# Kernel optimization log

Hardware: AMD Instinct MI355X
Metric: run time of the kernel (lower is better)

The kernel has to match this reference:

```python
import jax, jax.numpy as jnp
import numpy as np

B, S, H = 2, 2048, 2048
NH, NKV, HD = 16, 4, 128
THETA = 1000000.0

def _rope_tables(seq_len, dim, theta):
    inv_freq = 1.0 / (theta ** (np.arange(0, dim, 2, dtype=np.float32) / dim))
    t = np.arange(seq_len, dtype=np.float32)
    freqs = np.outer(t, inv_freq)                      # [S, dim/2]
    emb = np.concatenate([freqs, freqs], axis=-1)      # [S, dim]
    return jnp.asarray(np.cos(emb)), jnp.asarray(np.sin(emb))

def setup_inputs() -> dict:
    key = jax.random.key(0)
    ks = jax.random.split(key, 5)
    cos, sin = _rope_tables(S, HD, THETA)
    scale = 1.0 / np.sqrt(H)
    return {
        "x": jax.random.normal(ks[0], (B, S, H), jnp.float32),
        "cos": cos, "sin": sin,
        "wq": jax.random.normal(ks[1], (H, NH * HD), jnp.float32) * scale,
        "wk": jax.random.normal(ks[2], (H, NKV * HD), jnp.float32) * scale,
        "wv": jax.random.normal(ks[3], (H, NKV * HD), jnp.float32) * scale,
        "wo": jax.random.normal(ks[4], (NH * HD, H), jnp.float32) * scale,
    }

def _rotate_half(t):
    h = t.shape[-1] // 2
    return jnp.concatenate([-t[..., h:], t[..., :h]], axis=-1)

def reference(x, cos, sin, wq, wk, wv, wo):
    b, s, _ = x.shape
    n_rep = NH // NKV
    q = (x @ wq).reshape(b, s, NH, HD)    # [b,s,nh,hd]
    k = (x @ wk).reshape(b, s, NKV, HD)
    v = (x @ wv).reshape(b, s, NKV, HD)
    # RoPE: cos/sin [s,hd] broadcast over batch and heads
    c = cos[None, :, None, :]
    sn = sin[None, :, None, :]
    q = q * c + _rotate_half(q) * sn
    k = k * c + _rotate_half(k) * sn
    # GQA: repeat kv heads n_rep times
    k = jnp.repeat(k, n_rep, axis=2)      # [b,s,nh,hd]
    v = jnp.repeat(v, n_rep, axis=2)
    q = q.transpose(0, 2, 1, 3)           # [b,nh,s,hd]
    k = k.transpose(0, 2, 1, 3)
    v = v.transpose(0, 2, 1, 3)
    scores = jnp.einsum('bhqd,bhkd->bhqk', q, k) / jnp.sqrt(jnp.float32(HD))
    causal = jnp.tril(jnp.ones((s, s), dtype=bool))
    scores = jnp.where(causal[None, None], scores, jnp.float32(-jnp.inf))
    attn = jax.nn.softmax(scores.astype(jnp.float32), axis=-1).astype(q.dtype)
    out = jnp.einsum('bhqk,bhkd->bhqd', attn, v)
    out = out.transpose(0, 2, 1, 3).reshape(b, s, NH * HD)
    return out @ wo
```

## Files before the change

### kernel.cpp

```cpp
#include <hip/hip_runtime.h>
#include <hip/hip_bf16.h>

#define Bb 2
#define Ss 2048
#define Hh 2048
#define NH 16
#define NKV 4
#define HD 128
#define NREP (NH / NKV)
#define Mrows (Bb * Ss)
#define NQKV (NH*HD + 2*NKV*HD)

using short8 = __attribute__((ext_vector_type(8))) short;
using f32x4  = __attribute__((ext_vector_type(4))) float;

__device__ __forceinline__ unsigned short f2b(float f) {
  union { float f; unsigned u; } v; v.f = f;
  return (unsigned short)((v.u + 0x7fffu + ((v.u >> 16) & 1u)) >> 16);
}

__device__ __forceinline__ void gload16(const void* g, void* l) {
  __builtin_amdgcn_global_load_lds(
      (const __attribute__((address_space(1))) unsigned int*)g,
      (__attribute__((address_space(3))) unsigned int*)l, 16, 0, 0);
}

__global__ void cvt_bf16(const float* __restrict__ in, unsigned short* __restrict__ out, int n) {
  int i = (blockIdx.x * blockDim.x + threadIdx.x) * 4;
  if (i < n) {
    float4 f = *(const float4*)(in + i);
    ushort4 o;
    o.x = f2b(f.x); o.y = f2b(f.y); o.z = f2b(f.z); o.w = f2b(f.w);
    *(ushort4*)(out + i) = o;
  }
}

__global__ void transpose_cvt(const float* __restrict__ in, unsigned short* __restrict__ out,
                              int R, int C) {
  __shared__ float tile[32][33];
  int c0 = blockIdx.x * 32, r0 = blockIdx.y * 32;
  int tx = threadIdx.x, ty = threadIdx.y;
  #pragma unroll
  for (int i = ty; i < 32; i += 8)
    tile[i][tx] = in[(long)(r0 + i) * C + c0 + tx];
  __syncthreads();
  #pragma unroll
  for (int i = ty; i < 32; i += 8)
    out[(long)(c0 + i) * R + r0 + tx] = f2b(tile[tx][i]);
}

__global__ void transpose_qkv(const float* __restrict__ wq, const float* __restrict__ wk,
                              const float* __restrict__ wv, unsigned short* __restrict__ outT) {
  __shared__ float tile[32][33];
  int n0 = blockIdx.x * 32, k0 = blockIdx.y * 32;
  const float* src; int c0, C;
  if (n0 < Hh)            { src = wq; c0 = n0;            C = NH * HD; }
  else if (n0 < Hh + 512) { src = wk; c0 = n0 - Hh;       C = NKV * HD; }
  else                    { src = wv; c0 = n0 - Hh - 512; C = NKV * HD; }
  int tx = threadIdx.x, ty = threadIdx.y;
  #pragma unroll
  for (int i = ty; i < 32; i += 8)
    tile[i][tx] = src[(long)(k0 + i) * C + c0 + tx];
  __syncthreads();
  #pragma unroll
  for (int i = ty; i < 32; i += 8)
    outT[(long)(n0 + i) * Hh + k0 + tx] = f2b(tile[tx][i]);
}

__global__ __launch_bounds__(256) void gemm_qkv(const unsigned short* __restrict__ A,
                                                const unsigned short* __restrict__ Bt,
                                                const float* __restrict__ cosT,
                                                const float* __restrict__ sinT,
                                                unsigned short* __restrict__ qt,
                                                unsigned short* __restrict__ kt,
                                                unsigned short* __restrict__ vt) {
  __shared__ unsigned short As[128 * 32];
  __shared__ unsigned short Bs[128 * 32];
  const int t = threadIdx.x;
  const int lane = t & 63, wave = t >> 6;
  const int quad = lane >> 4, l16 = lane & 15;
  const int tile = blockIdx.x;
  const int n0 = tile * 128, m0 = blockIdx.y * 128;
  const int wm = wave * 32;
  const bool isv = tile >= 20;
  const int Kk = Hh;

  f32x4 acc[2][8] = {};

  const unsigned short* Ag0 = A + (long)(m0 + (t >> 2)) * Kk + (t & 3) * 8;
  const unsigned short* Ag1 = A + (long)(m0 + 64 + (t >> 2)) * Kk + (t & 3) * 8;
  const unsigned short* Bg0 = Bt + (long)(n0 + (t >> 2)) * Kk + (t & 3) * 8;
  const unsigned short* Bg1 = Bt + (long)(n0 + 64 + (t >> 2)) * Kk + (t & 3) * 8;
  unsigned short* lA0 = As + (wave * 64) * 8;
  unsigned short* lA1 = As + (wave * 64 + 256) * 8;
  unsigned short* lB0 = Bs + (wave * 64) * 8;
  unsigned short* lB1 = Bs + (wave * 64 + 256) * 8;

  for (int k0 = 0; k0 < Kk; k0 += 32) {
    gload16(Ag0 + k0, lA0);
    gload16(Ag1 + k0, lA1);
    gload16(Bg0 + k0, lB0);
    gload16(Bg1 + k0, lB1);
    __syncthreads();

    short8 af[2], bf[8];
    #pragma unroll
    for (int i = 0; i < 2; i++)
      af[i] = *(const short8*)(As + (wm + i * 16 + l16) * 32 + quad * 8);
    #pragma unroll
    for (int i = 0; i < 8; i++)
      bf[i] = *(const short8*)(Bs + (i * 16 + l16) * 32 + quad * 8);

    if (isv) {
      #pragma unroll
      for (int mi = 0; mi < 2; mi++)
        #pragma unroll
        for (int ni = 0; ni < 8; ni++)
          acc[mi][ni] = __builtin_amdgcn_mfma_f32_16x16x32_bf16(bf[ni], af[mi], acc[mi][ni], 0, 0, 0);
    } else {
      #pragma unroll
      for (int mi = 0; mi < 2; mi++)
        #pragma unroll
        for (int ni = 0; ni < 8; ni++)
          acc[mi][ni] = __builtin_amdgcn_mfma_f32_16x16x32_bf16(af[mi], bf[ni], acc[mi][ni], 0, 0, 0);
    }
    __syncthreads();
  }

  if (!isv) {
    const bool isq = tile < 16;
    const int hh = isq ? tile : tile - 16;
    #pragma unroll
    for (int mi = 0; mi < 2; mi++)
      #pragma unroll
      for (int r = 0; r < 4; r++) {
        int srow = m0 + wm + mi * 16 + quad * 4 + r;
        int bb = srow >> 11, s = srow & (Ss - 1);
        unsigned short* dst = isq ? qt + (((long)bb * NH + hh) * Ss + s) * HD
                                  : kt + (((long)bb * NKV + hh) * Ss + s) * HD;
        const float* cr = cosT + (long)s * HD;
        const float* sr = sinT + (long)s * HD;
        #pragma unroll
        for (int ni = 0; ni < 4; ni++) {
          int d = ni * 16 + l16;
          float cc = cr[d], sn = sr[d];
          float x0 = acc[mi][ni][r], x1 = acc[mi][ni + 4][r];
          dst[d]      = f2b(x0 * cc - x1 * sn);
          dst[d + 64] = f2b(x1 * cc + x0 * sn);
        }
      }
  } else {
    const int kvh = tile - 20;
    const int bb = m0 >> 11;
    #pragma unroll
    for (int mi = 0; mi < 2; mi++)
      #pragma unroll
      for (int ni = 0; ni < 8; ni++)
        #pragma unroll
        for (int r = 0; r < 4; r++) {
          int d = ni * 16 + quad * 4 + r;
          int s = (m0 + wm + mi * 16 + l16) & (Ss - 1);
          vt[(((long)bb * NKV + kvh) * HD + d) * Ss + s] = f2b(acc[mi][ni][r]);
        }
  }
}

__global__ __launch_bounds__(256) void gemm_bt(const unsigned short* __restrict__ A,
                                               const unsigned short* __restrict__ Bt,
                                               float* __restrict__ Cv,
                                               int Mm, int Nn, int Kk) {
  __shared__ unsigned short As[128 * 32];
  __shared__ unsigned short Bs[128 * 32];
  const int t = threadIdx.x;
  const int lane = t & 63, wave = t >> 6;
  const int quad = lane >> 4, l16 = lane & 15;
  const int m0 = blockIdx.y * 128, n0 = blockIdx.x * 128;
  const int wm = (wave >> 1) * 64, wn = (wave & 1) * 64;

  f32x4 acc[4][4] = {};

  const unsigned short* Ag0 = A + (long)(m0 + (t >> 2)) * Kk + (t & 3) * 8;
  const unsigned short* Ag1 = A + (long)(m0 + 64 + (t >> 2)) * Kk + (t & 3) * 8;
  const unsigned short* Bg0 = Bt + (long)(n0 + (t >> 2)) * Kk + (t & 3) * 8;
  const unsigned short* Bg1 = Bt + (long)(n0 + 64 + (t >> 2)) * Kk + (t & 3) * 8;
  unsigned short* lA0 = As + (wave * 64) * 8;
  unsigned short* lA1 = As + (wave * 64 + 256) * 8;
  unsigned short* lB0 = Bs + (wave * 64) * 8;
  unsigned short* lB1 = Bs + (wave * 64 + 256) * 8;

  for (int k0 = 0; k0 < Kk; k0 += 32) {
    gload16(Ag0 + k0, lA0);
    gload16(Ag1 + k0, lA1);
    gload16(Bg0 + k0, lB0);
    gload16(Bg1 + k0, lB1);
    __syncthreads();

    short8 af[4], bf[4];
    #pragma unroll
    for (int i = 0; i < 4; i++)
      af[i] = *(const short8*)(As + (wm + i * 16 + l16) * 32 + quad * 8);
    #pragma unroll
    for (int i = 0; i < 4; i++)
      bf[i] = *(const short8*)(Bs + (wn + i * 16 + l16) * 32 + quad * 8);

    #pragma unroll
    for (int mi = 0; mi < 4; mi++)
      #pragma unroll
      for (int ni = 0; ni < 4; ni++)
        acc[mi][ni] = __builtin_amdgcn_mfma_f32_16x16x32_bf16(af[mi], bf[ni], acc[mi][ni], 0, 0, 0);
    __syncthreads();
  }

  #pragma unroll
  for (int mi = 0; mi < 4; mi++)
    #pragma unroll
    for (int ni = 0; ni < 4; ni++)
      #pragma unroll
      for (int r = 0; r < 4; r++) {
        long row = m0 + wm + mi * 16 + quad * 4 + r;
        long col = n0 + wn + ni * 16 + l16;
        Cv[row * Nn + col] = acc[mi][ni][r];
      }
}

__global__ __launch_bounds__(256, 2) void flash_attn(const unsigned short* __restrict__ qt,
                                                     const unsigned short* __restrict__ kt,
                                                     const unsigned short* __restrict__ vt,
                                                     unsigned short* __restrict__ out) {
  __shared__ unsigned short Ks[2][64 * 128];
  __shared__ unsigned short Vs[2][128 * 64];

  const int w = threadIdx.x >> 6, lane = threadIdx.x & 63;
  const int quad = lane >> 4, l16 = lane & 15;
  const int r8 = lane >> 3, c8 = lane & 7;
  const int idx = blockIdx.x;
  const int t5 = idx >> 5;
  const int qblk = (idx < 256) ? (15 - t5) : (t5 - 8);
  const int bh = idx & 31;
  const int h = bh & (NH - 1), b = bh >> 4;
  const int q0w = qblk * 128 + w * 32;
  const int kvh = h / NREP;

  const unsigned short* Qb = qt + ((long)b * NH + h) * Ss * HD;
  const unsigned short* Kb = kt + ((long)b * NKV + kvh) * Ss * HD;
  const unsigned short* Vb = vt + ((long)b * NKV + kvh) * HD * Ss;
  const int nch = (qblk + 1) * 2;

  #pragma unroll
  for (int i = 0; i < 4; i++) {
    int rho = i * 16 + w * 4 + quad;
    int key = (rho & 32) + ((rho >> 2) & 3) * 8 + ((rho >> 4) & 1) * 4 + (rho & 3);
    int sg = l16 ^ (w * 4 + quad);
    gload16(Kb + (long)key * HD + sg * 8, &Ks[0][(i * 256 + w * 64) * 8]);
  }
  #pragma unroll
  for (int i = 0; i < 4; i++) {
    int dv = i * 32 + w * 8 + r8;
    int sg = c8 ^ r8;
    gload16(Vb + (long)dv * Ss + sg * 8, &Vs[0][(i * 256 + w * 64) * 8]);
  }

  short8 qf[2][4];
  #pragma unroll
  for (int qi = 0; qi < 2; qi++)
    #pragma unroll
    for (int kc = 0; kc < 4; kc++)
      qf[qi][kc] = *(const short8*)(Qb + (long)(q0w + qi * 16 + l16) * HD + kc * 32 + quad * 8);

  f32x4 accO[2][8] = {};
  float m_i[2], l_i[2];
  m_i[0] = m_i[1] = -__builtin_inff();
  l_i[0] = l_i[1] = 0.f;
  const float cscale = 1.4426950408889634f * 0.08838834764831845f;

  for (int c = 0; c < nch; ++c) {
    const unsigned short* Ksb = Ks[c & 1];
    const unsigned short* Vsb = Vs[c & 1];

    if (c + 1 < nch) {
      const int k0 = (c + 1) * 64;
      unsigned short* Kd = Ks[(c + 1) & 1];
      unsigned short* Vd = Vs[(c + 1) & 1];
      #pragma unroll
      for (int i = 0; i < 4; i++) {
        int rho = i * 16 + w * 4 + quad;
        int key = (rho & 32) + ((rho >> 2) & 3) * 8 + ((rho >> 4) & 1) * 4 + (rho & 3);
        int sg = l16 ^ (w * 4 + quad);
        gload16(Kb + (long)(k0 + key) * HD + sg * 8, Kd + (i * 256 + w * 64) * 8);
      }
      #pragma unroll
      for (int i = 0; i < 4; i++) {
        int dv = i * 32 + w * 8 + r8;
        int sg = c8 ^ r8;
        gload16(Vb + (long)dv * Ss + k0 + sg * 8, Vd + (i * 256 + w * 64) * 8);
      }
      asm volatile("s_waitcnt vmcnt(8)" ::: "memory");
    } else {
      asm volatile("s_waitcnt vmcnt(0)" ::: "memory");
    }
    asm volatile("s_barrier" ::: "memory");

    if (c * 64 < q0w + 32) {
      f32x4 sc[2][4] = {};
      #pragma unroll
      for (int T = 0; T < 4; T++)
        #pragma unroll
        for (int kc = 0; kc < 4; kc++) {
          short8 kf = *(const short8*)(Ksb + ((16 * T + l16) * 16 + ((kc * 4 + quad) ^ l16)) * 8);
          #pragma unroll
          for (int qi = 0; qi < 2; qi++)
            sc[qi][T] = __builtin_amdgcn_mfma_f32_16x16x32_bf16(kf, qf[qi][kc], sc[qi][T], 0, 0, 0);
        }

      if ((c + 1) * 64 - 1 > q0w) {
        #pragma unroll
        for (int qi = 0; qi < 2; qi++) {
          int qq = q0w + qi * 16 + l16;
          #pragma unroll
          for (int T = 0; T < 4; T++)
            #pragma unroll
            for (int r = 0; r < 4; r++) {
              int ka = c * 64 + (T >> 1) * 32 + quad * 8 + (T & 1) * 4 + r;
              if (ka > qq) sc[qi][T][r] = -__builtin_inff();
            }
        }
      }

      short8 pf[2][2];
      #pragma unroll
      for (int qi = 0; qi < 2; qi++) {
        float v = sc[qi][0][0];
        #pragma unroll
        for (int T = 0; T < 4; T++)
          #pragma unroll
          for (int r = 0; r < 4; r++) v = fmaxf(v, sc[qi][T][r]);
        v = fmaxf(v, __shfl_xor(v, 16));
        v = fmaxf(v, __shfl_xor(v, 32));
        float mn = fmaxf(m_i[qi], v);
        float alpha = __builtin_amdgcn_exp2f((m_i[qi] - mn) * cscale);
        m_i[qi] = mn;
        l_i[qi] *= alpha;
        #pragma unroll
        for (int Dt = 0; Dt < 8; Dt++)
          #pragma unroll
          for (int r = 0; r < 4; r++) accO[qi][Dt][r] *= alpha;

        float p[4][4], rs = 0.f;
        #pragma unroll
        for (int T = 0; T < 4; T++)
          #pragma unroll
          for (int r = 0; r < 4; r++) {
            p[T][r] = __builtin_amdgcn_exp2f((sc[qi][T][r] - mn) * cscale);
            rs += p[T][r];
          }
        rs += __shfl_xor(rs, 16);
        rs += __shfl_xor(rs, 32);
        l_i[qi] += rs;

        #pragma unroll
        for (int c2 = 0; c2 < 2; c2++) {
          short8 f;
          f[0] = (short)f2b(p[2 * c2][0]);     f[1] = (short)f2b(p[2 * c2][1]);
          f[2] = (short)f2b(p[2 * c2][2]);     f[3] = (short)f2b(p[2 * c2][3]);
          f[4] = (short)f2b(p[2 * c2 + 1][0]); f[5] = (short)f2b(p[2 * c2 + 1][1]);
          f[6] = (short)f2b(p[2 * c2 + 1][2]); f[7] = (short)f2b(p[2 * c2 + 1][3]);
          pf[qi][c2] = f;
        }
      }

      #pragma unroll
      for (int c2 = 0; c2 < 2; c2++)
        #pragma unroll
        for (int Dt = 0; Dt < 8; Dt++) {
          short8 vf = *(const short8*)(Vsb + ((16 * Dt + l16) * 8 + ((4 * c2 + quad) ^ (l16 & 7))) * 8);
          #pragma unroll
          for (int qi = 0; qi < 2; qi++)
            accO[qi][Dt] = __builtin_amdgcn_mfma_f32_16x16x32_bf16(vf, pf[qi][c2], accO[qi][Dt], 0, 0, 0);
        }
    }

    asm volatile("s_waitcnt lgkmcnt(0)" ::: "memory");
    asm volatile("s_barrier" ::: "memory");
  }

  #pragma unroll
  for (int qi = 0; qi < 2; qi++) {
    float inv = 1.f / l_i[qi];
    long orow = (long)b * Ss + q0w + qi * 16 + l16;
    #pragma unroll
    for (int Dt = 0; Dt < 8; Dt++) {
      ushort4 o;
      o.x = f2b(accO[qi][Dt][0] * inv);
      o.y = f2b(accO[qi][Dt][1] * inv);
      o.z = f2b(accO[qi][Dt][2] * inv);
      o.w = f2b(accO[qi][Dt][3] * inv);
      *(ushort4*)(out + orow * (NH * HD) + h * HD + Dt * 16 + quad * 4) = o;
    }
  }
}

extern "C" void kernel_launch(void* const* d_in, const int* in_sizes, int n_in,
                              void* d_out, int out_size, void* d_ws, size_t ws_size,
                              hipStream_t stream) {
  const float* x    = (const float*)d_in[0];
  const float* cosT = (const float*)d_in[1];
  const float* sinT = (const float*)d_in[2];
  const float* wq   = (const float*)d_in[3];
  const float* wk   = (const float*)d_in[4];
  const float* wv   = (const float*)d_in[5];
  const float* wo   = (const float*)d_in[6];
  float* out = (float*)d_out;

  char* ws = (char*)d_ws;
  unsigned short* xb    = (unsigned short*)(ws);
  unsigned short* wqkvt = (unsigned short*)(ws + (16l << 20));
  unsigned short* wot   = (unsigned short*)(ws + (28l << 20));
  unsigned short* qt    = (unsigned short*)(ws + (36l << 20));
  unsigned short* kt    = (unsigned short*)(ws + (52l << 20));
  unsigned short* vt    = (unsigned short*)(ws + (56l << 20));
  unsigned short* attno = xb;

  cvt_bf16<<<Mrows * Hh / 4 / 256, 256, 0, stream>>>(x, xb, Mrows * Hh);

  dim3 tb(32, 8);
  transpose_qkv<<<dim3(NQKV / 32, Hh / 32), tb, 0, stream>>>(wq, wk, wv, wqkvt);
  transpose_cvt<<<dim3(Hh / 32, Hh / 32), tb, 0, stream>>>(wo, wot, Hh, Hh);

  gemm_qkv<<<dim3(NQKV / 128, Mrows / 128), 256, 0, stream>>>(xb, wqkvt, cosT, sinT, qt, kt, vt);

  flash_attn<<<(Ss / 128) * NH * Bb, 256, 0, stream>>>(qt, kt, vt, attno);

  gemm_bt<<<dim3(Hh / 128, Mrows / 128), 256, 0, stream>>>(attno, wot, out, Mrows, Hh, Hh);
}
```

Baseline: 351.6 us.

## Double GEMM K-tile to 64 with XOR-swizzled LDS and column-major block order

Both bf16 GEMMs (QKV projection and output projection) now load a 64-wide K slice per iteration instead of 32. This halves the number of barrier pairs and global-load issue rounds. LDS rows are XOR-swizzled on 16-byte granules so the wider rows do not cause bank conflicts on the MFMA operand reads. The 2D grid is flattened so consecutive blocks walk down M for a fixed N tile, which is meant to improve L2 reuse of the weight tile. The cost is double the LDS per block (32 KB), which could lower occupancy.

```diff
diff --git a/kernel.cpp b/kernel.cpp
--- a/kernel.cpp
+++ b/kernel.cpp
@@ -74,55 +74,58 @@
                                                 unsigned short* __restrict__ qt,
                                                 unsigned short* __restrict__ kt,
                                                 unsigned short* __restrict__ vt) {
-  __shared__ unsigned short As[128 * 32];
-  __shared__ unsigned short Bs[128 * 32];
+  __shared__ unsigned short As[128 * 64];
+  __shared__ unsigned short Bs[128 * 64];
   const int t = threadIdx.x;
   const int lane = t & 63, wave = t >> 6;
   const int quad = lane >> 4, l16 = lane & 15;
-  const int tile = blockIdx.x;
-  const int n0 = tile * 128, m0 = blockIdx.y * 128;
+  const int tile = blockIdx.x >> 5;
+  const int n0 = tile * 128, m0 = (blockIdx.x & 31) * 128;
   const int wm = wave * 32;
   const bool isv = tile >= 20;
   const int Kk = Hh;
 
   f32x4 acc[2][8] = {};
 
-  const unsigned short* Ag0 = A + (long)(m0 + (t >> 2)) * Kk + (t & 3) * 8;
-  const unsigned short* Ag1 = A + (long)(m0 + 64 + (t >> 2)) * Kk + (t & 3) * 8;
-  const unsigned short* Bg0 = Bt + (long)(n0 + (t >> 2)) * Kk + (t & 3) * 8;
-  const unsigned short* Bg1 = Bt + (long)(n0 + 64 + (t >> 2)) * Kk + (t & 3) * 8;
-  unsigned short* lA0 = As + (wave * 64) * 8;
-  unsigned short* lA1 = As + (wave * 64 + 256) * 8;
-  unsigned short* lB0 = Bs + (wave * 64) * 8;
-  unsigned short* lB1 = Bs + (wave * 64 + 256) * 8;
-
-  for (int k0 = 0; k0 < Kk; k0 += 32) {
-    gload16(Ag0 + k0, lA0);
-    gload16(Ag1 + k0, lA1);
-    gload16(Bg0 + k0, lB0);
-    gload16(Bg1 + k0, lB1);
+  const int srow = t >> 3;
+  const int sgr  = (t & 7) ^ (srow & 7);
+  const unsigned short* Ag = A  + (long)(m0 + srow) * Kk + sgr * 8;
+  const unsigned short* Bg = Bt + (long)(n0 + srow) * Kk + sgr * 8;
+  unsigned short* lA = As + (wave * 64) * 8;
+  unsigned short* lB = Bs + (wave * 64) * 8;
+
+  for (int k0 = 0; k0 < Kk; k0 += 64) {
+    #pragma unroll
+    for (int i = 0; i < 4; i++)
+      gload16(Ag + (long)i * 32 * Kk + k0, lA + i * 256 * 8);
+    #pragma unroll
+    for (int i = 0; i < 4; i++)
+      gload16(Bg + (long)i * 32 * Kk + k0, lB + i * 256 * 8);
     __syncthreads();
 
-    short8 af[2], bf[8];
-    #pragma unroll
-    for (int i = 0; i < 2; i++)
-      af[i] = *(const short8*)(As + (wm + i * 16 + l16) * 32 + quad * 8);
-    #pragma unroll
-    for (int i = 0; i < 8; i++)
-      bf[i] = *(const short8*)(Bs + (i * 16 + l16) * 32 + quad * 8);
-
-    if (isv) {
-      #pragma unroll
-      for (int mi = 0; mi < 2; mi++)
-        #pragma unroll
-        for (int ni = 0; ni < 8; ni++)
-          acc[mi][ni] = __builtin_amdgcn_mfma_f32_16x16x32_bf16(bf[ni], af[mi], acc[mi][ni], 0, 0, 0);
-    } else {
-      #pragma unroll
-      for (int mi = 0; mi < 2; mi++)
-        #pragma unroll
-        for (int ni = 0; ni < 8; ni++)
-          acc[mi][ni] = __builtin_amdgcn_mfma_f32_16x16x32_bf16(af[mi], bf[ni], acc[mi][ni], 0, 0, 0);
+    #pragma unroll
+    for (int sub = 0; sub < 2; sub++) {
+      short8 af[2], bf[8];
+      #pragma unroll
+      for (int i = 0; i < 2; i++)
+        af[i] = *(const short8*)(As + (wm + i * 16 + l16) * 64 + (((sub * 4 + quad) ^ (l16 & 7)) * 8));
+      #pragma unroll
+      for (int i = 0; i < 8; i++)
+        bf[i] = *(const short8*)(Bs + (i * 16 + l16) * 64 + (((sub * 4 + quad) ^ (l16 & 7)) * 8));
+
+      if (isv) {
+        #pragma unroll
+        for (int mi = 0; mi < 2; mi++)
+          #pragma unroll
+          for (int ni = 0; ni < 8; ni++)
+            acc[mi][ni] = __builtin_amdgcn_mfma_f32_16x16x32_bf16(bf[ni], af[mi], acc[mi][ni], 0, 0, 0);
+      } else {
+        #pragma unroll
+        for (int mi = 0; mi < 2; mi++)
+          #pragma unroll
+          for (int ni = 0; ni < 8; ni++)
+            acc[mi][ni] = __builtin_amdgcn_mfma_f32_16x16x32_bf16(af[mi], bf[ni], acc[mi][ni], 0, 0, 0);
+      }
     }
     __syncthreads();
   }
@@ -134,8 +137,8 @@
     for (int mi = 0; mi < 2; mi++)
       #pragma unroll
       for (int r = 0; r < 4; r++) {
-        int srow = m0 + wm + mi * 16 + quad * 4 + r;
-        int bb = srow >> 11, s = srow & (Ss - 1);
+        int srw = m0 + wm + mi * 16 + quad * 4 + r;
+        int bb = srw >> 11, s = srw & (Ss - 1);
         unsigned short* dst = isq ? qt + (((long)bb * NH + hh) * Ss + s) * HD
                                   : kt + (((long)bb * NKV + hh) * Ss + s) * HD;
         const float* cr = cosT + (long)s * HD;
@@ -169,45 +172,48 @@
                                                const unsigned short* __restrict__ Bt,
                                                float* __restrict__ Cv,
                                                int Mm, int Nn, int Kk) {
-  __shared__ unsigned short As[128 * 32];
-  __shared__ unsigned short Bs[128 * 32];
+  __shared__ unsigned short As[128 * 64];
+  __shared__ unsigned short Bs[128 * 64];
   const int t = threadIdx.x;
   const int lane = t & 63, wave = t >> 6;
   const int quad = lane >> 4, l16 = lane & 15;
-  const int m0 = blockIdx.y * 128, n0 = blockIdx.x * 128;
+  const int n0 = (blockIdx.x >> 5) * 128, m0 = (blockIdx.x & 31) * 128;
   const int wm = (wave >> 1) * 64, wn = (wave & 1) * 64;
 
   f32x4 acc[4][4] = {};
 
-  const unsigned short* Ag0 = A + (long)(m0 + (t >> 2)) * Kk + (t & 3) * 8;
-  const unsigned short* Ag1 = A + (long)(m0 + 64 + (t >> 2)) * Kk + (t & 3) * 8;
-  const unsigned short* Bg0 = Bt + (long)(n0 + (t >> 2)) * Kk + (t & 3) * 8;
-  const unsigned short* Bg1 = Bt + (long)(n0 + 64 + (t >> 2)) * Kk + (t & 3) * 8;
-  unsigned short* lA0 = As + (wave * 64) * 8;
-  unsigned short* lA1 = As + (wave * 64 + 256) * 8;
-  unsigned short* lB0 = Bs + (wave * 64) * 8;
-  unsigned short* lB1 = Bs + (wave * 64 + 256) * 8;
-
-  for (int k0 = 0; k0 < Kk; k0 += 32) {
-    gload16(Ag0 + k0, lA0);
-    gload16(Ag1 + k0, lA1);
-    gload16(Bg0 + k0, lB0);
-    gload16(Bg1 + k0, lB1);
+  const int srow = t >> 3;
+  const int sgr  = (t & 7) ^ (srow & 7);
+  const unsigned short* Ag = A  + (long)(m0 + srow) * Kk + sgr * 8;
+  const unsigned short* Bg = Bt + (long)(n0 + srow) * Kk + sgr * 8;
+  unsigned short* lA = As + (wave * 64) * 8;
+  unsigned short* lB = Bs + (wave * 64) * 8;
+
+  for (int k0 = 0; k0 < Kk; k0 += 64) {
+    #pragma unroll
+    for (int i = 0; i < 4; i++)
+      gload16(Ag + (long)i * 32 * Kk + k0, lA + i * 256 * 8);
+    #pragma unroll
+    for (int i = 0; i < 4; i++)
+      gload16(Bg + (long)i * 32 * Kk + k0, lB + i * 256 * 8);
     __syncthreads();
 
-    short8 af[4], bf[4];
-    #pragma unroll
-    for (int i = 0; i < 4; i++)
-      af[i] = *(const short8*)(As + (wm + i * 16 + l16) * 32 + quad * 8);
-    #pragma unroll
-    for (int i = 0; i < 4; i++)
-      bf[i] = *(const short8*)(Bs + (wn + i * 16 + l16) * 32 + quad * 8);
-
-    #pragma unroll
-    for (int mi = 0; mi < 4; mi++)
-      #pragma unroll
-      for (int ni = 0; ni < 4; ni++)
-        acc[mi][ni] = __builtin_amdgcn_mfma_f32_16x16x32_bf16(af[mi], bf[ni], acc[mi][ni], 0, 0, 0);
+    #pragma unroll
+    for (int sub = 0; sub < 2; sub++) {
+      short8 af[4], bf[4];
+      #pragma unroll
+      for (int i = 0; i < 4; i++)
+        af[i] = *(const short8*)(As + (wm + i * 16 + l16) * 64 + (((sub * 4 + quad) ^ (l16 & 7)) * 8));
+      #pragma unroll
+      for (int i = 0; i < 4; i++)
+        bf[i] = *(const short8*)(Bs + (wn + i * 16 + l16) * 64 + (((sub * 4 + quad) ^ (l16 & 7)) * 8));
+
+      #pragma unroll
+      for (int mi = 0; mi < 4; mi++)
+        #pragma unroll
+        for (int ni = 0; ni < 4; ni++)
+          acc[mi][ni] = __builtin_amdgcn_mfma_f32_16x16x32_bf16(af[mi], bf[ni], acc[mi][ni], 0, 0, 0);
+    }
     __syncthreads();
   }
 
@@ -426,9 +432,9 @@
   transpose_qkv<<<dim3(NQKV / 32, Hh / 32), tb, 0, stream>>>(wq, wk, wv, wqkvt);
   transpose_cvt<<<dim3(Hh / 32, Hh / 32), tb, 0, stream>>>(wo, wot, Hh, Hh);
 
-  gemm_qkv<<<dim3(NQKV / 128, Mrows / 128), 256, 0, stream>>>(xb, wqkvt, cosT, sinT, qt, kt, vt);
+  gemm_qkv<<<(NQKV / 128) * (Mrows / 128), 256, 0, stream>>>(xb, wqkvt, cosT, sinT, qt, kt, vt);
 
   flash_attn<<<(Ss / 128) * NH * Bb, 256, 0, stream>>>(qt, kt, vt, attno);
 
-  gemm_bt<<<dim3(Hh / 128, Mrows / 128), 256, 0, stream>>>(attno, wot, out, Mrows, Hh, Hh);
-}
+  gemm_bt<<<(Hh / 128) * (Mrows / 128), 256, 0, stream>>>(attno, wot, out, Mrows, Hh, Hh);
+}
```

Result: faster. 321.0 us (-8.7%).
